# Kernel tuning notes

Measured on AMD Instinct MI355X. Metric: run time of the kernel, lower is better.

## Reference

```python
import jax, jax.numpy as jnp
import numpy as np

B, T, C, L = 512, 512, 96, 64   # batch, time steps, num classes (incl. blank), max label len
BLANK = C - 1                   # keras ctc_batch_cost uses last class as blank
EPS = 1e-7                      # epsilon added before log, as in ctc_batch_cost
NEG = -1e30                     # log-space -inf surrogate


def setup_inputs():
    key = jax.random.key(0)
    k1, k2, k3 = jax.random.split(key, 3)
    # y_pred is a softmax output: positive, rows sum to 1
    u = jax.random.uniform(k1, (B, T, C), dtype=jnp.float32, minval=0.1, maxval=1.0)
    y_pred = u / jnp.sum(u, axis=-1, keepdims=True)
    # labels in [0, BLANK), variable lengths, padded with -1 (as the layer expects)
    labels = jax.random.randint(k2, (B, L), 0, C - 1, dtype=jnp.int32)
    lens = jax.random.randint(k3, (B,), L // 2, L + 1, dtype=jnp.int32)
    y_true = jnp.where(jnp.arange(L)[None, :] < lens[:, None], labels, -1)
    return {"y_true": y_true, "y_pred": y_pred}


def _ctc_loss(y_true, y_pred):
    """Per-example CTC negative log-likelihood (forward DP in log space)."""
    y_true = y_true.astype(jnp.int32)
    lbl_len = jnp.sum((y_true != -1).astype(jnp.int32), axis=-1)          # (B,)
    labels = jnp.where(y_true != -1, y_true, 0)                            # (B,L)

    S = 2 * L + 1
    # extended label: blank, l0, blank, l1, ..., blank
    ext = jnp.full((B, S), BLANK, dtype=jnp.int32).at[:, 1::2].set(labels)  # (B,S)
    ext_m2 = jnp.pad(ext[:, :-2], ((0, 0), (2, 0)), constant_values=BLANK)
    can_skip = (ext != BLANK) & (ext != ext_m2)                             # (B,S)

    lp = jnp.log(y_pred.astype(jnp.float32) + EPS)   # (B,T,C) log-probs
    lp_t = jnp.swapaxes(lp, 0, 1)                    # (T,B,C) for scan over time

    emit0 = jnp.take_along_axis(lp_t[0], ext, axis=1)                       # (B,S)
    alpha0 = (jnp.full((B, S), NEG, dtype=jnp.float32)
              .at[:, 0].set(emit0[:, 0])
              .at[:, 1].set(emit0[:, 1]))

    def step(alpha, lpt):
        a1 = jnp.pad(alpha[:, :-1], ((0, 0), (1, 0)), constant_values=NEG)
        a2 = jnp.pad(alpha[:, :-2], ((0, 0), (2, 0)), constant_values=NEG)
        a2 = jnp.where(can_skip, a2, NEG)
        m = jnp.maximum(alpha, jnp.maximum(a1, a2))
        lse = m + jnp.log(jnp.exp(alpha - m) + jnp.exp(a1 - m) + jnp.exp(a2 - m))
        alpha_new = lse + jnp.take_along_axis(lpt, ext, axis=1)
        return alpha_new, None

    alphaT, _ = jax.lax.scan(step, alpha0, lp_t[1:])

    # total log-prob ends at last blank (s=2*len) or last label (s=2*len-1)
    i_blank = (2 * lbl_len)[:, None]
    i_label = jnp.maximum(2 * lbl_len - 1, 0)[:, None]
    a_b = jnp.take_along_axis(alphaT, i_blank, axis=1)[:, 0]
    a_l = jnp.take_along_axis(alphaT, i_label, axis=1)[:, 0]
    return -jnp.logaddexp(a_b, a_l)                                         # (B,)


def reference(y_true, y_pred):
    # layer adds tf.reduce_mean(ctc_batch_cost(...)) as the model loss
    return jnp.mean(_ctc_loss(y_true, y_pred))
```

## Files before the change

### kernel.cpp

```cpp
#include <hip/hip_runtime.h>


#define B_ 512
#define T_ 512
#define C_ 96
#define L_ 64
#define BLANK_ 95
#define EPSF 1e-7f
#define LN2F 0.69314718055994530942f

template <int CTRL>
__device__ __forceinline__ float dpp_mov(float x) {
    return __int_as_float(
        __builtin_amdgcn_update_dpp(0, __float_as_int(x), CTRL, 0xF, 0xF, true));
}

__device__ __forceinline__ float wave_max(float m) {
    m = fmaxf(m, dpp_mov<0x111>(m));
    m = fmaxf(m, dpp_mov<0x112>(m));
    m = fmaxf(m, dpp_mov<0x114>(m));
    m = fmaxf(m, dpp_mov<0x118>(m));
    m = fmaxf(m, dpp_mov<0x142>(m));
    m = fmaxf(m, dpp_mov<0x143>(m));
    return __int_as_float(__builtin_amdgcn_readlane(__float_as_int(m), 63));
}

__launch_bounds__(64, 1)
__global__ void ctc_loss_kernel(const int* __restrict__ y_true,
                                const float* __restrict__ y_pred,
                                float* __restrict__ out) {
    const int b = blockIdx.x;
    const int lane = threadIdx.x;

    const int yv = y_true[b * L_ + lane];
    const unsigned long long act = __ballot(yv != -1);
    const int len = __popcll(act);
    const int lab = (yv == -1) ? 0 : yv;
    const int lab_prev = __shfl_up(lab, 1);
    const bool cs = (lane == 0) ? true : (lab != lab_prev);

    const float* rowp = y_pred + (size_t)b * T_ * C_;
    const float* plp = rowp + lab;
    const float* pbp = rowp + BLANK_;

    constexpr int U = 8;
    constexpr int NCH = T_ / U;
    float bl[3][U], bb[3][U];
#pragma unroll
    for (int d = 0; d < 3; ++d)
#pragma unroll
        for (int k = 0; k < U; ++k) {
            bl[d][k] = plp[(d * U + k) * C_];
            bb[d][k] = pbp[(d * U + k) * C_];
        }

    float a_even, a_odd, a128;
    int accum = 0;
    {
        const float pb0 = bb[0][0] + EPSF;
        const float pl0 = bl[0][0] + EPSF;
        a_even = (lane == 0) ? pb0 : 0.0f;
        a_odd  = (lane == 0) ? pl0 : 0.0f;
        a128 = 0.0f;
    }

    auto step = [&](float rl, float rb) {
        const float pbv = rb + EPSF;
        const float plv = rl + EPSF;
        const float po = dpp_mov<0x138>(a_odd);
        const float pos = cs ? po : 0.0f;
        const float ne = (a_even + po) * pbv;
        const float no = (a_odd + a_even + pos) * plv;
        a128 = (a128 + a_odd) * pbv;
        a_even = ne;
        a_odd = no;
    };

    auto renorm = [&]() {
        const float mv = wave_max(fmaxf(fmaxf(a_even, a_odd), a128));
        const int e = ((__float_as_int(mv) >> 23) & 0xFF) - 126;
        const int k = 96 - e;
        a_even = ldexpf(a_even, k);
        a_odd  = ldexpf(a_odd, k);
        a128   = ldexpf(a128, k);
        accum -= k;
    };

    auto prefetch = [&](float* dl, float* db, int t0) {
#pragma unroll
        for (int k = 0; k < U; ++k) {
            dl[k] = plp[(t0 + k) * C_];
            db[k] = pbp[(t0 + k) * C_];
        }
    };

#pragma unroll
    for (int k = 1; k < U; ++k) step(bl[0][k], bb[0][k]);
    renorm();
    prefetch(bl[0], bb[0], 3 * U);

    for (int g = 0; g < 21; ++g) {
        const int cbase = 1 + g * 3;
#pragma unroll
        for (int sub = 0; sub < 3; ++sub) {
            const int slot = (sub + 1) % 3;
#pragma unroll
            for (int k = 0; k < U; ++k) step(bl[slot][k], bb[slot][k]);
            renorm();
            const int pc = cbase + sub + 3;
            if (pc < NCH) prefetch(bl[slot], bb[slot], pc * U);
        }
    }

    const float al = __shfl(a_odd, len - 1);
    const float ab = (len < L_) ? __shfl(a_even, len)
                                : __shfl(a128, 63);
    if (lane == 0) {
        const float loss = -LN2F * (log2f(ab + al) + (float)accum);
        atomicAdd(out, loss * (1.0f / B_));
    }
}

extern "C" void kernel_launch(void* const* d_in, const int* in_sizes, int n_in,
                              void* d_out, int out_size, void* d_ws, size_t ws_size,
                              hipStream_t stream) {
    const int* y_true = (const int*)d_in[0];
    const float* y_pred = (const float*)d_in[1];
    float* out = (float*)d_out;
    hipMemsetAsync(out, 0, sizeof(float), stream);
    ctc_loss_kernel<<<B_, 64, 0, stream>>>(y_true, y_pred, out);
}
```

Baseline: 157.4 us.

## Stage emission rows through LDS with coalesced float4 loads and 4-deep register prefetch

Replaces the per-lane strided scalar gathers of the label and blank probabilities with coalesced float4 loads of whole 16-timestep chunks of y_pred. Each chunk is written into a double-buffered shared-memory tile, and every lane then reads its own label and blank emissions from that tile. Four chunks are kept in flight in registers to hide global latency. This trades many uncoalesced 4-byte loads per lane for full-row coalesced traffic. The cost is reading all 96 classes, extra LDS traffic, and more register pressure (96 extra VGPRs for the prefetch buffers).

```diff
diff --git a/kernel.cpp b/kernel.cpp
--- a/kernel.cpp
+++ b/kernel.cpp
@@ -8,6 +8,10 @@
 #define BLANK_ 95
 #define EPSF 1e-7f
 #define LN2F 0.69314718055994530942f
+#define U_ 16
+#define CHF_ (U_ * C_)
+
+template <int N> struct Ic { static constexpr int v = N; };
 
 template <int CTRL>
 __device__ __forceinline__ float dpp_mov(float x) {
@@ -29,6 +33,7 @@
 __global__ void ctc_loss_kernel(const int* __restrict__ y_true,
                                 const float* __restrict__ y_pred,
                                 float* __restrict__ out) {
+    __shared__ alignas(16) float smem[2][CHF_];
     const int b = blockIdx.x;
     const int lane = threadIdx.x;
 
@@ -39,34 +44,35 @@
     const int lab_prev = __shfl_up(lab, 1);
     const bool cs = (lane == 0) ? true : (lab != lab_prev);
 
-    const float* rowp = y_pred + (size_t)b * T_ * C_;
-    const float* plp = rowp + lab;
-    const float* pbp = rowp + BLANK_;
+    const float4* g4 = (const float4*)(y_pred + (size_t)b * (T_ * C_));
 
-    constexpr int U = 8;
-    constexpr int NCH = T_ / U;
-    float bl[3][U], bb[3][U];
-#pragma unroll
-    for (int d = 0; d < 3; ++d)
-#pragma unroll
-        for (int k = 0; k < U; ++k) {
-            bl[d][k] = plp[(d * U + k) * C_];
-            bb[d][k] = pbp[(d * U + k) * C_];
-        }
-
+    float4 rb[4][6];
+    float el[U_], eb[U_];
     float a_even, a_odd, a128;
     int accum = 0;
-    {
-        const float pb0 = bb[0][0] + EPSF;
-        const float pl0 = bl[0][0] + EPSF;
-        a_even = (lane == 0) ? pb0 : 0.0f;
-        a_odd  = (lane == 0) ? pl0 : 0.0f;
-        a128 = 0.0f;
-    }
 
-    auto step = [&](float rl, float rb) {
-        const float pbv = rb + EPSF;
-        const float plv = rl + EPSF;
+    auto load_chunk = [&](auto BK_, int c) {
+        constexpr int BK = decltype(BK_)::v;
+        const float4* g = g4 + c * (CHF_ / 4) + lane;
+#pragma unroll
+        for (int i = 0; i < 6; ++i) rb[BK][i] = g[i * 64];
+    };
+    auto store_chunk = [&](auto BK_, auto SL_) {
+        constexpr int BK = decltype(BK_)::v;
+        float4* s = (float4*)&smem[decltype(SL_)::v][0];
+#pragma unroll
+        for (int i = 0; i < 6; ++i) s[i * 64 + lane] = rb[BK][i];
+    };
+    auto read_emis = [&](auto SL_) {
+        constexpr int SL = decltype(SL_)::v;
+#pragma unroll
+        for (int k = 0; k < U_; ++k) {
+            el[k] = smem[SL][k * C_ + lab] + EPSF;
+            eb[k] = smem[SL][k * C_ + BLANK_] + EPSF;
+        }
+    };
+
+    auto step = [&](float plv, float pbv) {
         const float po = dpp_mov<0x138>(a_odd);
         const float pos = cs ? po : 0.0f;
         const float ne = (a_even + po) * pbv;
@@ -86,31 +92,52 @@
         accum -= k;
     };
 
-    auto prefetch = [&](float* dl, float* db, int t0) {
+    auto body = [&](auto CB_, int c, auto LD_) {
+        constexpr int CB = decltype(CB_)::v;
+        constexpr int SL = CB & 1;
+        store_chunk(Ic<CB>{}, Ic<SL>{});
+        if constexpr (decltype(LD_)::v) load_chunk(Ic<CB>{}, c + 4);
+        read_emis(Ic<SL>{});
 #pragma unroll
-        for (int k = 0; k < U; ++k) {
-            dl[k] = plp[(t0 + k) * C_];
-            db[k] = pbp[(t0 + k) * C_];
-        }
+        for (int k = 0; k < 8; ++k) step(el[k], eb[k]);
+        renorm();
+#pragma unroll
+        for (int k = 8; k < U_; ++k) step(el[k], eb[k]);
+        renorm();
     };
 
+    load_chunk(Ic<0>{}, 0);
+    load_chunk(Ic<1>{}, 1);
+    load_chunk(Ic<2>{}, 2);
+    load_chunk(Ic<3>{}, 3);
+
+    store_chunk(Ic<0>{}, Ic<0>{});
+    load_chunk(Ic<0>{}, 4);
+    read_emis(Ic<0>{});
+    a_even = (lane == 0) ? eb[0] : 0.0f;
+    a_odd  = (lane == 0) ? el[0] : 0.0f;
+    a128 = 0.0f;
 #pragma unroll
-    for (int k = 1; k < U; ++k) step(bl[0][k], bb[0][k]);
+    for (int k = 1; k < 8; ++k) step(el[k], eb[k]);
     renorm();
-    prefetch(bl[0], bb[0], 3 * U);
+#pragma unroll
+    for (int k = 8; k < U_; ++k) step(el[k], eb[k]);
+    renorm();
 
-    for (int g = 0; g < 21; ++g) {
-        const int cbase = 1 + g * 3;
-#pragma unroll
-        for (int sub = 0; sub < 3; ++sub) {
-            const int slot = (sub + 1) % 3;
-#pragma unroll
-            for (int k = 0; k < U; ++k) step(bl[slot][k], bb[slot][k]);
-            renorm();
-            const int pc = cbase + sub + 3;
-            if (pc < NCH) prefetch(bl[slot], bb[slot], pc * U);
-        }
+    for (int g = 0; g < 6; ++g) {
+        const int c0 = 1 + g * 4;
+        body(Ic<1>{}, c0 + 0, Ic<1>{});
+        body(Ic<2>{}, c0 + 1, Ic<1>{});
+        body(Ic<3>{}, c0 + 2, Ic<1>{});
+        body(Ic<0>{}, c0 + 3, Ic<1>{});
     }
+    body(Ic<1>{}, 25, Ic<1>{});
+    body(Ic<2>{}, 26, Ic<1>{});
+    body(Ic<3>{}, 27, Ic<1>{});
+    body(Ic<0>{}, 28, Ic<0>{});
+    body(Ic<1>{}, 29, Ic<0>{});
+    body(Ic<2>{}, 30, Ic<0>{});
+    body(Ic<3>{}, 31, Ic<0>{});
 
     const float al = __shfl(a_odd, len - 1);
     const float ab = (len < L_) ? __shfl(a_even, len)
```

Measured after the change: 289.2 us. 83.8% more time.

## Stage y_pred chunks through LDS with coalesced float4 loads and double buffering

Applied to the files above, without the earlier changes.

Replaces the per-lane strided scalar gathers of label and blank probabilities with coalesced float4 loads of whole 32-timestep chunks into registers. Each chunk is written to a double-buffered shared-memory array, and the emission values are gathered from LDS. Global loads for chunk c+2 are issued while chunk c is processed, so memory latency is hidden behind the serial DP. The trade-off is 24 KB of LDS per block, 12 float4 staging registers plus 64 emission registers, and reading every class instead of only two per lane. Since the wave is 64 threads, no barrier is used.

```diff
diff --git a/kernel.cpp b/kernel.cpp
--- a/kernel.cpp
+++ b/kernel.cpp
@@ -8,6 +8,9 @@
 #define BLANK_ 95
 #define EPSF 1e-7f
 #define LN2F 0.69314718055994530942f
+#define U_ 32
+#define CHF_ (U_ * C_)
+#define NCH_ (T_ / U_)
 
 template <int CTRL>
 __device__ __forceinline__ float dpp_mov(float x) {
@@ -29,6 +32,7 @@
 __global__ void ctc_loss_kernel(const int* __restrict__ y_true,
                                 const float* __restrict__ y_pred,
                                 float* __restrict__ out) {
+    __shared__ alignas(16) float smem[2][CHF_];
     const int b = blockIdx.x;
     const int lane = threadIdx.x;
 
@@ -39,34 +43,35 @@
     const int lab_prev = __shfl_up(lab, 1);
     const bool cs = (lane == 0) ? true : (lab != lab_prev);
 
-    const float* rowp = y_pred + (size_t)b * T_ * C_;
-    const float* plp = rowp + lab;
-    const float* pbp = rowp + BLANK_;
+    const float4* g4 = (const float4*)(y_pred + (size_t)b * (T_ * C_));
 
-    constexpr int U = 8;
-    constexpr int NCH = T_ / U;
-    float bl[3][U], bb[3][U];
-#pragma unroll
-    for (int d = 0; d < 3; ++d)
-#pragma unroll
-        for (int k = 0; k < U; ++k) {
-            bl[d][k] = plp[(d * U + k) * C_];
-            bb[d][k] = pbp[(d * U + k) * C_];
-        }
-
+    float4 s0, s1, s2, s3, s4, s5, s6, s7, s8, s9, s10, s11;
+    float el[U_], eb[U_];
     float a_even, a_odd, a128;
     int accum = 0;
-    {
-        const float pb0 = bb[0][0] + EPSF;
-        const float pl0 = bl[0][0] + EPSF;
-        a_even = (lane == 0) ? pb0 : 0.0f;
-        a_odd  = (lane == 0) ? pl0 : 0.0f;
-        a128 = 0.0f;
-    }
 
-    auto step = [&](float rl, float rb) {
-        const float pbv = rb + EPSF;
-        const float plv = rl + EPSF;
+    auto load_chunk = [&](int c) {
+        const float4* g = g4 + c * (CHF_ / 4) + lane;
+        s0 = g[0 * 64];  s1 = g[1 * 64];  s2 = g[2 * 64];  s3 = g[3 * 64];
+        s4 = g[4 * 64];  s5 = g[5 * 64];  s6 = g[6 * 64];  s7 = g[7 * 64];
+        s8 = g[8 * 64];  s9 = g[9 * 64];  s10 = g[10 * 64]; s11 = g[11 * 64];
+    };
+    auto store_chunk = [&](int sl) {
+        float4* s = (float4*)&smem[sl][0] + lane;
+        s[0 * 64] = s0;  s[1 * 64] = s1;  s[2 * 64] = s2;  s[3 * 64] = s3;
+        s[4 * 64] = s4;  s[5 * 64] = s5;  s[6 * 64] = s6;  s[7 * 64] = s7;
+        s[8 * 64] = s8;  s[9 * 64] = s9;  s[10 * 64] = s10; s[11 * 64] = s11;
+    };
+    auto read_emis = [&](int sl) {
+        const float* base = &smem[sl][0];
+#pragma unroll
+        for (int k = 0; k < U_; ++k) {
+            el[k] = base[k * C_ + lab] + EPSF;
+            eb[k] = base[k * C_ + BLANK_] + EPSF;
+        }
+    };
+
+    auto step = [&](float plv, float pbv) {
         const float po = dpp_mov<0x138>(a_odd);
         const float pos = cs ? po : 0.0f;
         const float ne = (a_even + po) * pbv;
@@ -86,30 +91,41 @@
         accum -= k;
     };
 
-    auto prefetch = [&](float* dl, float* db, int t0) {
+    auto body = [&](int c, bool ld) {
+        read_emis(c & 1);
+        store_chunk((c + 1) & 1);
+        if (ld) load_chunk(c + 2);
 #pragma unroll
-        for (int k = 0; k < U; ++k) {
-            dl[k] = plp[(t0 + k) * C_];
-            db[k] = pbp[(t0 + k) * C_];
+        for (int k = 0; k < U_; ++k) {
+            step(el[k], eb[k]);
+            if ((k & 7) == 7) renorm();
         }
     };
 
+    load_chunk(0);
+    store_chunk(0);
+    load_chunk(1);
+    read_emis(0);
+
+    store_chunk(1);
+    load_chunk(2);
+    a_even = (lane == 0) ? eb[0] : 0.0f;
+    a_odd  = (lane == 0) ? el[0] : 0.0f;
+    a128 = 0.0f;
 #pragma unroll
-    for (int k = 1; k < U; ++k) step(bl[0][k], bb[0][k]);
-    renorm();
-    prefetch(bl[0], bb[0], 3 * U);
+    for (int k = 1; k < U_; ++k) {
+        step(el[k], eb[k]);
+        if ((k & 7) == 7) renorm();
+    }
 
-    for (int g = 0; g < 21; ++g) {
-        const int cbase = 1 + g * 3;
+    for (int c = 1; c <= 13; ++c) body(c, true);
+    body(14, false);
+
+    read_emis(1);
 #pragma unroll
-        for (int sub = 0; sub < 3; ++sub) {
-            const int slot = (sub + 1) % 3;
-#pragma unroll
-            for (int k = 0; k < U; ++k) step(bl[slot][k], bb[slot][k]);
-            renorm();
-            const int pc = cbase + sub + 3;
-            if (pc < NCH) prefetch(bl[slot], bb[slot], pc * U);
-        }
+    for (int k = 0; k < U_; ++k) {
+        step(el[k], eb[k]);
+        if ((k & 7) == 7) renorm();
     }
 
     const float al = __shfl(a_odd, len - 1);
```

After: 153.0 us. 2.8% less time.
